# Optimization experiments

Measured on AMD Instinct MI355X. Metric: run time of the kernel, lower is better.

## Reference

```python
import jax, jax.numpy as jnp
import numpy as np

T = 16384      # trajectory length
Z = 8          # num_zones
DIN = 8        # person_attrs_dim
E = 16         # num edges
PENALTY = 1000.0
DIFFUSION_STRENGTH = 0.2
EPS = 1e-20


def setup_inputs() -> dict:
    key = jax.random.key(0)
    ks = jax.random.split(key, 20)
    s = 0.05  # weight scale
    return {
        "person_attrs": jax.random.normal(ks[0], (DIN,), jnp.float32),
        "times": jnp.arange(T, dtype=jnp.float32),
        "gumbel_u": jax.random.uniform(ks[1], (T, Z), jnp.float32),
        "edge_index": jax.random.randint(ks[2], (2, E), 0, Z),
        "W1": jax.random.normal(ks[3], (256, DIN + 1 + Z), jnp.float32) * s,
        "b1": jnp.zeros((256,), jnp.float32),
        "W2": jax.random.normal(ks[4], (128, 256), jnp.float32) * s,
        "b2": jnp.zeros((128,), jnp.float32),
        "W3": jax.random.normal(ks[5], (64, 128), jnp.float32) * s,
        "b3": jnp.zeros((64,), jnp.float32),
        "W4": jax.random.normal(ks[6], (Z, 64), jnp.float32) * s,
        "b4": jnp.zeros((Z,), jnp.float32),
        "D1": jax.random.normal(ks[7], (128, DIN + 1), jnp.float32) * s,
        "d1": jnp.zeros((128,), jnp.float32),
        "D2": jax.random.normal(ks[8], (64, 128), jnp.float32) * s,
        "d2": jnp.zeros((64,), jnp.float32),
        "D3": jax.random.normal(ks[9], (Z, 64), jnp.float32) * s,
        "d3": jnp.zeros((Z,), jnp.float32),
        "tau": jnp.asarray(1.0, jnp.float32),
    }


def _adjacency(edge_index, num_zones):
    A = jnp.zeros((num_zones, num_zones), jnp.float32)
    A = A.at[edge_index[0], edge_index[1]].set(1.0)
    A = A.at[edge_index[1], edge_index[0]].set(1.0)
    d = jnp.arange(num_zones)
    return A.at[d, d].set(1.0)


def _forward(person_attrs, times, gumbel_u, W1, b1, W2, b2, W3, b3, W4, b4,
             D1, d1, D2, d2, D3, d3, tau, edge_index):
    num_zones = W4.shape[0]
    din = person_attrs.shape[0]
    A = _adjacency(edge_index, num_zones)

    # normalized time: times / times[-1] if times[-1] > 0 else 0
    last = times[-1]
    denom = jnp.where(last > 0, last, jnp.asarray(1.0, times.dtype))
    norm_t = jnp.where(last > 0, times / denom, jnp.zeros_like(times))  # [T]

    # Precompute (attrs, time)-dependent parts batched over all timesteps.
    # trajectory_net layer 1 split: columns [0:din]=attrs, [din]=time, [din+1:]=zone one-hot
    f_base = person_attrs @ W1[:, :din].T + norm_t[:, None] * W1[:, din][None, :] + b1  # [T,256]
    W1z = W1[:, din + 1:]  # [256, Z]

    # diversity_net depends only on (attrs, time): batch it fully.
    h = jax.nn.relu(person_attrs @ D1[:, :din].T + norm_t[:, None] * D1[:, din][None, :] + d1)  # [T,128]
    h = jax.nn.relu(h @ D2.T + d2)                                                              # [T,64]
    diversity = jnp.tanh(h @ D3.T + d3)                                                         # [T,Z]

    gumbels = -jnp.log(-jnp.log(gumbel_u + EPS) + EPS)  # [T,Z]

    zone0 = jax.nn.one_hot(0, num_zones, dtype=jnp.float32)

    def step(zone_soft, xs):
        f1, dv, g = xs
        h1 = jax.nn.relu(f1 + W1z @ zone_soft)
        h2 = jax.nn.relu(W2 @ h1 + b2)
        h3 = jax.nn.relu(W3 @ h2 + b3)
        base_logits = W4 @ h3 + b4
        combined = base_logits + DIFFUSION_STRENGTH * dv
        cur = jnp.argmax(zone_soft)
        constrained = combined - PENALTY * (1.0 - A[cur])
        y = jax.nn.softmax((constrained + g) / tau)
        nxt = jnp.argmax(y)
        hard = jax.nn.one_hot(nxt, num_zones, dtype=y.dtype)
        zone_next = y + jax.lax.stop_gradient(hard - y)  # straight-through hard gumbel
        return zone_next, (constrained, nxt)

    _, (traj_logits, traj_zones) = jax.lax.scan(step, zone0, (f_base, diversity, gumbels))
    return traj_logits, traj_zones


def reference(person_attrs, times, gumbel_u, edge_index, W1, b1, W2, b2, W3, b3,
              W4, b4, D1, d1, D2, d2, D3, d3, tau):
    return _forward(person_attrs, times, gumbel_u, W1, b1, W2, b2, W3, b3, W4, b4,
                    D1, d1, D2, d2, D3, d3, tau, edge_index)
```

## Files before the change

### kernel.cpp

```cpp
#include <hip/hip_runtime.h>
#include <cstdint>

#define T_STEPS 16384

#define WS_U     0
#define WS_V     256
#define WS_W1ZT  512
#define WS_PEN   2560
#define WS_A     2624
#define WS_W4T   2688
#define WS_W2T   3968
#define WS_W3T   36736
#define WS_DV    53120
#define WS_G     184192
#define WS_CONS  315264
#define WS_ABT   1363840
#define WS_A4LR  1888128
#define WS_H3LR  1920896
#define WS_END_F 2183040
#define WSB_NXT8 ((size_t)WS_END_F * 4)
#define WSB_CUR  (WSB_NXT8 + 131072)
#define WSB_CRX  (WSB_CUR + 65536)

#define PB_DIV   0
#define PB_W2T   256
#define PB_W3T   (PB_W2T + 128)
#define PB_GUM   (PB_W3T + 32)
#define PB_SETUP (PB_GUM + 512)
#define NB_PREP  (PB_SETUP + 1)

__device__ __forceinline__ unsigned int fn_compose(unsigned int hi, unsigned int lo) {
  unsigned int r = 0;
  #pragma unroll
  for (int x = 0; x < 8; ++x) {
    unsigned int m = (lo >> (3 * x)) & 7u;
    r |= ((hi >> (3 * m)) & 7u) << (3 * x);
  }
  return r;
}

__global__ void __launch_bounds__(256) k_prepdiv(
    const float* __restrict__ pa, const float* __restrict__ times,
    const float* __restrict__ gum, const int* __restrict__ edge,
    const float* __restrict__ W1, const float* __restrict__ b1,
    const float* __restrict__ W2, const float* __restrict__ W3,
    const float* __restrict__ W4,
    const float* __restrict__ D1, const float* __restrict__ d1,
    const float* __restrict__ D2, const float* __restrict__ d2,
    const float* __restrict__ D3, const float* __restrict__ d3,
    float* __restrict__ ws) {
  __shared__ float sD2[64 * 128];
  __shared__ float sudc[128], svdc[128];
  __shared__ float part[3][8][64];
  int b = blockIdx.x, tid = threadIdx.x;
  if (b < PB_W2T) {
    int lane = tid & 63;
    int w = __builtin_amdgcn_readfirstlane(tid >> 6);
    int t = b * 64 + lane;
    float last = times[T_STEPS - 1];
    float st = (last > 0.0f) ? times[t] / last : 0.0f;
    #pragma unroll
    for (int i = 0; i < 8; ++i)
      ((float4*)sD2)[i * 256 + tid] = ((const float4*)D2)[i * 256 + tid];
    if (tid < 128) {
      float acc = d1[tid];
      #pragma unroll
      for (int i = 0; i < 8; ++i) acc = fmaf(pa[i], D1[tid * 9 + i], acc);
      sudc[tid] = acc;
      svdc[tid] = D1[tid * 9 + 8];
    }
    __syncthreads();
    int j0 = __builtin_amdgcn_readfirstlane(w * 16);
    float accj[16];
    #pragma unroll
    for (int jj = 0; jj < 16; ++jj) accj[jj] = d2[j0 + jj];
    #pragma unroll 4
    for (int k = 0; k < 128; ++k) {
      float h1 = fmaxf(fmaf(st, svdc[k], sudc[k]), 0.0f);
      #pragma unroll
      for (int jj = 0; jj < 16; ++jj)
        accj[jj] = fmaf(sD2[(j0 + jj) * 128 + k], h1, accj[jj]);
    }
    float dvp[8];
    #pragma unroll
    for (int z = 0; z < 8; ++z) dvp[z] = (w == 0) ? d3[z] : 0.0f;
    #pragma unroll
    for (int jj = 0; jj < 16; ++jj) {
      float h2 = fmaxf(accj[jj], 0.0f);
      #pragma unroll
      for (int z = 0; z < 8; ++z)
        dvp[z] = fmaf(D3[z * 64 + j0 + jj], h2, dvp[z]);
    }
    if (w > 0) {
      #pragma unroll
      for (int z = 0; z < 8; ++z) part[w - 1][z][lane] = dvp[z];
    }
    __syncthreads();
    if (w == 0) {
      #pragma unroll
      for (int z = 0; z < 8; ++z) {
        float dvv = dvp[z] + part[0][z][lane] + part[1][z][lane] + part[2][z][lane];
        ws[WS_DV + t * 8 + z] = tanhf(dvv);
      }
    }
  } else if (b < PB_W3T) {
    int e = (b - PB_W2T) * 256 + tid;
    int k = e >> 7, j = e & 127;
    ws[WS_W2T + e] = W2[j * 256 + k];
  } else if (b < PB_GUM) {
    int e = (b - PB_W3T) * 256 + tid;
    int i = e & 63, j = e >> 6;
    ws[WS_W3T + e] = W3[i * 128 + j];
  } else if (b < PB_SETUP) {
    int e = (b - PB_GUM) * 256 + tid;
    float uu = gum[e];
    ws[WS_G + e] = -logf(-logf(uu + 1e-20f) + 1e-20f);
  } else {
    {
      int k = tid;
      float acc = b1[k];
      #pragma unroll
      for (int i = 0; i < 8; ++i) acc = fmaf(pa[i], W1[k * 17 + i], acc);
      ws[WS_U + k] = acc;
      ws[WS_V + k] = W1[k * 17 + 8];
    }
    for (int e = tid; e < 2048; e += 256) {
      int cc = e >> 8, k = e & 255;
      ws[WS_W1ZT + e] = W1[k * 17 + 9 + cc];
    }
    for (int e = tid; e < 512; e += 256) {
      int k = e >> 3, z = e & 7;
      ws[WS_W4T + e] = W4[z * 64 + k];
    }
    if (tid < 64) ws[WS_A + tid] = ((tid >> 3) == (tid & 7)) ? 1.0f : 0.0f;
    __syncthreads();
    if (tid == 0) {
      for (int e = 0; e < 16; ++e) {
        int aa = edge[e], bb = edge[16 + e];
        ws[WS_A + aa * 8 + bb] = 1.0f;
        ws[WS_A + bb * 8 + aa] = 1.0f;
      }
    }
    __syncthreads();
    if (tid < 64) ws[WS_PEN + tid] = 1000.0f * (1.0f - ws[WS_A + tid]);
  }
}

__global__ void __launch_bounds__(256) k_ab4(
    const float* __restrict__ times,
    const float* __restrict__ u_, const float* __restrict__ v_,
    const float* __restrict__ w1zt, const float* __restrict__ w2t,
    const float* __restrict__ w3t, const float* __restrict__ w4t,
    const float* __restrict__ b2, const float* __restrict__ b3,
    const float* __restrict__ b4,
    float* __restrict__ abt, int* __restrict__ crx,
    float* __restrict__ a4lr, float* __restrict__ h3lr) {
  __shared__ float s_au[256], s_av[256];
  __shared__ float s_pa[128], s_pb[128];
  __shared__ unsigned long long s_bal[4];
  __shared__ unsigned long long s_bal2[2];
  __shared__ float s_h2L[128], s_h2R[128];
  __shared__ float s_h3pL[4][64], s_h3pR[4][64];
  __shared__ float s_h3L[64], s_h3R[64];
  __shared__ int s_d3, s_cnt, s_cnt2;
  int blk = blockIdx.x;
  int c = blk >> 8, tile = blk & 255;
  int tid = threadIdx.x;
  float last = times[T_STEPS - 1];
  float stL = (last > 0.0f) ? times[tile * 64] / last : 0.0f;
  float stR = (last > 0.0f) ? times[tile * 64 + 63] / last : 0.0f;
  {
    float uk = u_[tid] + w1zt[c * 256 + tid];
    float vk = v_[tid];
    float valL = fmaf(stL, vk, uk);
    float valR = fmaf(stR, vk, uk);
    float mn = fminf(valL, valR);
    float mx = fmaxf(valL, valR);
    bool act = (mn > 0.0f);
    bool cross = (!act) && (mx > 0.0f);
    s_au[tid] = act ? uk : 0.0f;
    s_av[tid] = act ? vk : 0.0f;
    unsigned long long bal = __ballot(cross);
    if ((tid & 63) == 0) s_bal[tid >> 6] = bal;
  }
  if (tid == 0) s_d3 = 0;
  __syncthreads();
  if (tid == 0) {
    int cnt = 0;
    int list8[8];
    #pragma unroll
    for (int i = 0; i < 8; ++i) list8[i] = 0;
    #pragma unroll
    for (int w = 0; w < 4; ++w) {
      unsigned long long m = s_bal[w];
      while (m) {
        int bit = __ffsll(m) - 1;
        if (cnt < 8) list8[cnt] = w * 64 + bit;
        ++cnt;
        m &= (m - 1);
      }
    }
    crx[blk * 24] = cnt;
    s_cnt = cnt;
    #pragma unroll
    for (int i = 0; i < 8; ++i) crx[blk * 24 + 1 + i] = list8[i];
  }
  {
    int j = tid & 127, half = tid >> 7;
    float A = 0.0f, B = 0.0f;
    const float* wrow = w2t + half * 128 * 128 + j;
    int kb = half * 128;
    #pragma unroll 4
    for (int kk = 0; kk < 128; ++kk) {
      float w = wrow[kk * 128];
      A = fmaf(s_au[kb + kk], w, A);
      B = fmaf(s_av[kb + kk], w, B);
    }
    if (half == 1) { s_pa[j] = A; s_pb[j] = B; }
    __syncthreads();
    bool jcross = false;
    if (half == 0) {
      float Af = A + s_pa[j] + b2[j];
      float Bf = B + s_pb[j];
      abt[(size_t)blk * 256 + j * 2]     = Af;
      abt[(size_t)blk * 256 + j * 2 + 1] = Bf;
      float preL = fmaf(stL, Bf, Af);
      float preR = fmaf(stR, Bf, Af);
      jcross = (preL > 0.0f) != (preR > 0.0f);
      s_h2L[j] = fmaxf(preL, 0.0f);
      s_h2R[j] = fmaxf(preR, 0.0f);
    }
    unsigned long long bal2 = __ballot(jcross);
    if ((tid & 63) == 0 && tid < 128) s_bal2[tid >> 6] = bal2;
  }
  __syncthreads();
  if (tid == 0) {
    int cnt2 = 0;
    int list8[8];
    #pragma unroll
    for (int i = 0; i < 8; ++i) list8[i] = 0;
    #pragma unroll
    for (int w = 0; w < 2; ++w) {
      unsigned long long m = s_bal2[w];
      while (m) {
        int bit = __ffsll(m) - 1;
        if (cnt2 < 8) list8[cnt2] = w * 64 + bit;
        ++cnt2;
        m &= (m - 1);
      }
    }
    crx[blk * 24 + 10] = cnt2;
    s_cnt2 = cnt2;
    #pragma unroll
    for (int i = 0; i < 8; ++i) crx[blk * 24 + 11 + i] = list8[i];
  }
  __syncthreads();
  {
    int i = tid & 63, jq = tid >> 6;
    float aL = (jq == 0) ? b3[i] : 0.0f;
    float aR = aL;
    int j0 = jq * 32;
    #pragma unroll 4
    for (int jj = 0; jj < 32; ++jj) {
      float w = w3t[(j0 + jj) * 64 + i];
      aL = fmaf(w, s_h2L[j0 + jj], aL);
      aR = fmaf(w, s_h2R[j0 + jj], aR);
    }
    s_h3pL[jq][i] = aL;
    s_h3pR[jq][i] = aR;
  }
  __syncthreads();
  if (tid < 64) {
    float preL = s_h3pL[0][tid] + s_h3pL[1][tid] + s_h3pL[2][tid] + s_h3pL[3][tid];
    float preR = s_h3pR[0][tid] + s_h3pR[1][tid] + s_h3pR[2][tid] + s_h3pR[3][tid];
    if ((preL > 0.0f) != (preR > 0.0f)) atomicOr(&s_d3, 1);
    s_h3L[tid] = fmaxf(preL, 0.0f);
    s_h3R[tid] = fmaxf(preR, 0.0f);
    h3lr[(size_t)blk * 128 + tid]      = preL;
    h3lr[(size_t)blk * 128 + 64 + tid] = preR;
  }
  __syncthreads();
  if (tid < 8) {
    float aL = b4[tid], aR = b4[tid];
    #pragma unroll 8
    for (int i = 0; i < 64; ++i) {
      float w = w4t[i * 8 + tid];
      aL = fmaf(w, s_h3L[i], aL);
      aR = fmaf(w, s_h3R[i], aR);
    }
    a4lr[blk * 16 + tid]     = aL;
    a4lr[blk * 16 + 8 + tid] = aR;
  }
  if (tid == 0) {
    int flag;
    if (s_cnt > 0 || s_cnt2 > 8) flag = 0;
    else if (s_cnt2 > 0 || s_d3) flag = 3;
    else flag = 1;
    crx[blk * 24 + 9] = flag;
  }
}

__global__ void __launch_bounds__(256, 4) k_mlp(
    const float* __restrict__ times,
    const float* __restrict__ u_, const float* __restrict__ v_,
    const float* __restrict__ w1zt, const float* __restrict__ w2t,
    const float* __restrict__ abt, const int* __restrict__ crx,
    const float* __restrict__ a4lr, const float* __restrict__ h3lr,
    const float* __restrict__ w3t, const float* __restrict__ w4t,
    const float* __restrict__ b2, const float* __restrict__ b3,
    const float* __restrict__ b4,
    const float* __restrict__ dv, const float* __restrict__ gt,
    const float* __restrict__ pen, const float* __restrict__ tau,
    float* __restrict__ cons_out, unsigned char* __restrict__ nxt_out) {
  __shared__ float part[3][8][64];
  __shared__ float s_w3[8192];
  __shared__ float s_ab[256];
  int tid = threadIdx.x;
  int lane = tid & 63;
  int iq = __builtin_amdgcn_readfirstlane(tid >> 6);
  int blk = blockIdx.x;
  int c = blk >> 8, tgrp = blk & 255;
  int t = tgrp * 64 + lane;
  int abase = blk * 256;
  int cbase = blk * 24;
  int flag = crx[cbase + 9];

  if (flag == 1) {
    if (iq == 0) {
      float frac = (float)lane * (1.0f / 63.0f);
      float a4[8];
      #pragma unroll
      for (int z = 0; z < 8; ++z) {
        float L = a4lr[blk * 16 + z];
        float R = a4lr[blk * 16 + 8 + z];
        a4[z] = fmaf(frac, R - L, L);
      }
      float4 dv0 = *(const float4*)(dv + (size_t)t * 8);
      float4 dv1 = *(const float4*)(dv + (size_t)t * 8 + 4);
      float4 g0  = *(const float4*)(gt + (size_t)t * 8);
      float4 g1  = *(const float4*)(gt + (size_t)t * 8 + 4);
      float dvv[8] = {dv0.x, dv0.y, dv0.z, dv0.w, dv1.x, dv1.y, dv1.z, dv1.w};
      float gv[8]  = {g0.x, g0.y, g0.z, g0.w, g1.x, g1.y, g1.z, g1.w};
      float sgn = (tau[0] > 0.0f) ? 1.0f : -1.0f;
      float cons[8];
      float best = 0.0f; int bz = 0;
      #pragma unroll
      for (int z = 0; z < 8; ++z) {
        float lg = fmaf(0.2f, dvv[z], a4[z]) - pen[c * 8 + z];
        cons[z] = lg;
        float yv = (lg + gv[z]) * sgn;
        if (z == 0) { best = yv; bz = 0; }
        else if (yv > best) { best = yv; bz = z; }
      }
      float* co = cons_out + ((size_t)t * 8 + c) * 8;
      *(float4*)co = make_float4(cons[0], cons[1], cons[2], cons[3]);
      *(float4*)(co + 4) = make_float4(cons[4], cons[5], cons[6], cons[7]);
      nxt_out[t * 8 + c] = (unsigned char)bz;
    }
    return;
  }

  float last = times[T_STEPS - 1];
  float st = (last > 0.0f) ? times[t] / last : 0.0f;
  const float* w1c = w1zt + c * 256;
  int cnt = crx[cbase];
  int i0 = iq * 16;

  float acc[16];
  if (flag == 3) {
    float frac = (float)lane * (1.0f / 63.0f);
    #pragma unroll
    for (int i = 0; i < 16; ++i) {
      float L = h3lr[(size_t)blk * 128 + i0 + i];
      float R = h3lr[(size_t)blk * 128 + 64 + i0 + i];
      acc[i] = fmaf(frac, R - L, L);
    }
    int cnt2 = crx[cbase + 10];
    float stL = (last > 0.0f) ? times[tgrp * 64] / last : 0.0f;
    float stR = (last > 0.0f) ? times[tgrp * 64 + 63] / last : 0.0f;
    for (int q = 0; q < cnt2; ++q) {
      int j = crx[cbase + 11 + q];
      float A = abt[abase + j * 2];
      float B = abt[abase + j * 2 + 1];
      float preL = fmaf(stL, B, A);
      float preR = fmaf(stR, B, A);
      float rL = fmaxf(preL, 0.0f);
      float rR = fmaxf(preR, 0.0f);
      float pre = fmaf(st, B, A);
      float corr = fmaxf(pre, 0.0f) - fmaf(frac, rR - rL, rL);
      #pragma unroll
      for (int i = 0; i < 16; ++i)
        acc[i] = fmaf(corr, w3t[j * 64 + i0 + i], acc[i]);
    }
  } else {
    {
      const float4* w3v = (const float4*)w3t;
      float4* sw3 = (float4*)s_w3;
      #pragma unroll
      for (int r = 0; r < 8; ++r) sw3[r * 256 + tid] = w3v[r * 256 + tid];
      s_ab[tid] = abt[abase + tid];
    }
    __syncthreads();
    #pragma unroll
    for (int i = 0; i < 16; ++i) acc[i] = b3[i0 + i];

    if (cnt <= 8) {
      int kk[8];
      #pragma unroll
      for (int i = 0; i < 8; ++i) kk[i] = (i < cnt) ? crx[cbase + 1 + i] : 0;
      float hx[8];
      #pragma unroll
      for (int i = 0; i < 8; ++i)
        hx[i] = (i < cnt) ? fmaxf(fmaf(st, v_[kk[i]], u_[kk[i]] + w1c[kk[i]]), 0.0f) : 0.0f;
      #pragma unroll 2
      for (int j = 0; j < 128; ++j) {
        float2 ab = *(const float2*)(s_ab + j * 2);
        float h2p = fmaf(st, ab.y, ab.x);
        #pragma unroll
        for (int i = 0; i < 8; ++i)
          h2p = fmaf(hx[i], w2t[kk[i] * 128 + j], h2p);
        float h2 = fmaxf(h2p, 0.0f);
        const float4* w3p = (const float4*)(s_w3 + j * 64 + i0);
        float4 w0 = w3p[0], w1 = w3p[1], w2v = w3p[2], w3v = w3p[3];
        acc[0]  = fmaf(w0.x, h2, acc[0]);   acc[1]  = fmaf(w0.y, h2, acc[1]);
        acc[2]  = fmaf(w0.z, h2, acc[2]);   acc[3]  = fmaf(w0.w, h2, acc[3]);
        acc[4]  = fmaf(w1.x, h2, acc[4]);   acc[5]  = fmaf(w1.y, h2, acc[5]);
        acc[6]  = fmaf(w1.z, h2, acc[6]);   acc[7]  = fmaf(w1.w, h2, acc[7]);
        acc[8]  = fmaf(w2v.x, h2, acc[8]);  acc[9]  = fmaf(w2v.y, h2, acc[9]);
        acc[10] = fmaf(w2v.z, h2, acc[10]); acc[11] = fmaf(w2v.w, h2, acc[11]);
        acc[12] = fmaf(w3v.x, h2, acc[12]); acc[13] = fmaf(w3v.y, h2, acc[13]);
        acc[14] = fmaf(w3v.z, h2, acc[14]); acc[15] = fmaf(w3v.w, h2, acc[15]);
      }
    } else {
      for (int j = 0; j < 128; ++j) {
        float h2p = b2[j];
        for (int k = 0; k < 256; ++k) {
          float h1 = fmaxf(fmaf(st, v_[k], u_[k] + w1c[k]), 0.0f);
          h2p = fmaf(w2t[k * 128 + j], h1, h2p);
        }
        float h2 = fmaxf(h2p, 0.0f);
        #pragma unroll
        for (int i = 0; i < 16; ++i)
          acc[i] = fmaf(s_w3[j * 64 + i0 + i], h2, acc[i]);
      }
    }
  }

  float p[8];
  #pragma unroll
  for (int z = 0; z < 8; ++z) p[z] = (iq == 0) ? b4[z] : 0.0f;
  #pragma unroll 4
  for (int i = 0; i < 16; ++i) {
    float h3 = fmaxf(acc[i], 0.0f);
    #pragma unroll
    for (int z = 0; z < 8; ++z)
      p[z] = fmaf(w4t[(i0 + i) * 8 + z], h3, p[z]);
  }
  if (iq > 0) {
    #pragma unroll
    for (int z = 0; z < 8; ++z) part[iq - 1][z][lane] = p[z];
  }
  __syncthreads();
  if (iq == 0) {
    float a4[8];
    #pragma unroll
    for (int z = 0; z < 8; ++z)
      a4[z] = p[z] + part[0][z][lane] + part[1][z][lane] + part[2][z][lane];
    float4 dv0 = *(const float4*)(dv + (size_t)t * 8);
    float4 dv1 = *(const float4*)(dv + (size_t)t * 8 + 4);
    float4 g0  = *(const float4*)(gt + (size_t)t * 8);
    float4 g1  = *(const float4*)(gt + (size_t)t * 8 + 4);
    float dvv[8] = {dv0.x, dv0.y, dv0.z, dv0.w, dv1.x, dv1.y, dv1.z, dv1.w};
    float gv[8]  = {g0.x, g0.y, g0.z, g0.w, g1.x, g1.y, g1.z, g1.w};
    float sgn = (tau[0] > 0.0f) ? 1.0f : -1.0f;
    float cons[8];
    float best = 0.0f; int bz = 0;
    #pragma unroll
    for (int z = 0; z < 8; ++z) {
      float lg = fmaf(0.2f, dvv[z], a4[z]) - pen[c * 8 + z];
      cons[z] = lg;
      float yv = (lg + gv[z]) * sgn;
      if (z == 0) { best = yv; bz = 0; }
      else if (yv > best) { best = yv; bz = z; }
    }
    float* co = cons_out + ((size_t)t * 8 + c) * 8;
    *(float4*)co = make_float4(cons[0], cons[1], cons[2], cons[3]);
    *(float4*)(co + 4) = make_float4(cons[4], cons[5], cons[6], cons[7]);
    nxt_out[t * 8 + c] = (unsigned char)bz;
  }
}

__global__ void __launch_bounds__(1024) k_scangather(const float* __restrict__ ws,
                                                     float* __restrict__ d_out) {
  __shared__ unsigned int sc[1024];
  __shared__ unsigned char cur_s[128];
  int tid = threadIdx.x;
  int bid = blockIdx.x;
  const unsigned char* nxt8 = (const unsigned char*)ws + WSB_NXT8;
  const unsigned int IDENT = 0x00FAC688u;
  unsigned int f[16];
  int t0 = tid * 16;
  unsigned int F = IDENT;
  #pragma unroll
  for (int i = 0; i < 16; ++i) {
    uint2 b = *(const uint2*)(nxt8 + (size_t)(t0 + i) * 8);
    unsigned int fn = 0;
    #pragma unroll
    for (int q = 0; q < 4; ++q) fn |= ((b.x >> (8 * q)) & 7u) << (3 * q);
    #pragma unroll
    for (int q = 0; q < 4; ++q) fn |= ((b.y >> (8 * q)) & 7u) << (3 * (q + 4));
    f[i] = fn;
    F = fn_compose(fn, F);
  }
  sc[tid] = F;
  __syncthreads();
  #pragma unroll
  for (int d = 1; d < 1024; d <<= 1) {
    unsigned int v = sc[tid];
    unsigned int p = (tid >= d) ? sc[tid - d] : 0u;
    unsigned int nv = (tid >= d) ? fn_compose(v, p) : v;
    __syncthreads();
    sc[tid] = nv;
    __syncthreads();
  }
  unsigned int E = (tid == 0) ? IDENT : sc[tid - 1];
  unsigned int state = E & 7u;
  bool mine = (tid >> 3) == bid;
  #pragma unroll
  for (int i = 0; i < 16; ++i) {
    int tt = t0 + i;
    unsigned int nx = (f[i] >> (3 * state)) & 7u;
    if (mine) {
      cur_s[tt - bid * 128] = (unsigned char)state;
      d_out[131072 + tt] = (float)nx;
    }
    state = nx;
  }
  __syncthreads();
  int idx = bid * 1024 + tid;
  int t = idx >> 3, z = idx & 7;
  unsigned int cur = cur_s[t - bid * 128];
  d_out[idx] = ws[WS_CONS + ((size_t)t * 8 + (int)cur) * 8 + z];
}

extern "C" void kernel_launch(void* const* d_in, const int* in_sizes, int n_in,
                              void* d_out, int out_size, void* d_ws, size_t ws_size,
                              hipStream_t stream) {
  const float* pa    = (const float*)d_in[0];
  const float* times = (const float*)d_in[1];
  const float* gum   = (const float*)d_in[2];
  const int*   edge  = (const int*)d_in[3];
  const float* W1  = (const float*)d_in[4];
  const float* b1  = (const float*)d_in[5];
  const float* W2  = (const float*)d_in[6];
  const float* b2  = (const float*)d_in[7];
  const float* W3  = (const float*)d_in[8];
  const float* b3  = (const float*)d_in[9];
  const float* W4  = (const float*)d_in[10];
  const float* b4  = (const float*)d_in[11];
  const float* D1  = (const float*)d_in[12];
  const float* d1v = (const float*)d_in[13];
  const float* D2  = (const float*)d_in[14];
  const float* d2v = (const float*)d_in[15];
  const float* D3  = (const float*)d_in[16];
  const float* d3v = (const float*)d_in[17];
  const float* tau = (const float*)d_in[18];
  float* ws = (float*)d_ws;
  float* out = (float*)d_out;
  int* crx = (int*)((char*)d_ws + WSB_CRX);

  k_prepdiv<<<NB_PREP, 256, 0, stream>>>(pa, times, gum, edge, W1, b1, W2, W3, W4,
                                         D1, d1v, D2, d2v, D3, d3v, ws);
  k_ab4<<<2048, 256, 0, stream>>>(times, ws + WS_U, ws + WS_V, ws + WS_W1ZT,
                                  ws + WS_W2T, ws + WS_W3T, ws + WS_W4T,
                                  b2, b3, b4, ws + WS_ABT, crx,
                                  ws + WS_A4LR, ws + WS_H3LR);
  k_mlp<<<2048, 256, 0, stream>>>(times, ws + WS_U, ws + WS_V, ws + WS_W1ZT,
                                  ws + WS_W2T, ws + WS_ABT, crx,
                                  ws + WS_A4LR, ws + WS_H3LR,
                                  ws + WS_W3T, ws + WS_W4T, b2, b3, b4,
                                  ws + WS_DV, ws + WS_G, ws + WS_PEN, tau,
                                  ws + WS_CONS, (unsigned char*)ws + WSB_NXT8);
  k_scangather<<<128, 1024, 0, stream>>>(ws, out);
}
```

Measured before the change: 79.15 us.

## Move diversity and gumbel work into ab kernel; recompute linear-tile logits in gather

The diversity MLP and the gumbel transform move out of the small prep kernel into the large ab kernel as extra blocks, sharing shared memory through a union, and the D2 staging is split into two halves to cut LDS use. This shortens the serial prep launch and lets that work overlap with the ab tiles. The fast linear-tile path in the MLP kernel no longer writes the full 8x8 constrained logits per step. The gather kernel instead rebuilds the needed row from the tile endpoint logits, the diversity term and the penalty when the tile flag says the tile is linear. This trades a large write for extra reads and branching in the final gather.

```diff
diff --git a/kernel.cpp b/kernel.cpp
--- a/kernel.cpp
+++ b/kernel.cpp
@@ -19,15 +19,13 @@
 #define WS_H3LR  1920896
 #define WS_END_F 2183040
 #define WSB_NXT8 ((size_t)WS_END_F * 4)
-#define WSB_CUR  (WSB_NXT8 + 131072)
-#define WSB_CRX  (WSB_CUR + 65536)
-
-#define PB_DIV   0
-#define PB_W2T   256
-#define PB_W3T   (PB_W2T + 128)
-#define PB_GUM   (PB_W3T + 32)
-#define PB_SETUP (PB_GUM + 512)
-#define NB_PREP  (PB_SETUP + 1)
+#define WSB_CRX  (WSB_NXT8 + 131072 + 65536)
+
+#define NB_PREP  161
+#define AB_N     2048
+#define DIVB     2048
+#define GUMB     (DIVB + 256)
+#define NB_ABDG  (GUMB + 512)
 
 __device__ __forceinline__ unsigned int fn_compose(unsigned int hi, unsigned int lo) {
   unsigned int r = 0;
@@ -39,82 +37,21 @@
   return r;
 }
 
-__global__ void __launch_bounds__(256) k_prepdiv(
-    const float* __restrict__ pa, const float* __restrict__ times,
-    const float* __restrict__ gum, const int* __restrict__ edge,
+__global__ void __launch_bounds__(256) k_prep(
+    const float* __restrict__ pa, const int* __restrict__ edge,
     const float* __restrict__ W1, const float* __restrict__ b1,
     const float* __restrict__ W2, const float* __restrict__ W3,
     const float* __restrict__ W4,
-    const float* __restrict__ D1, const float* __restrict__ d1,
-    const float* __restrict__ D2, const float* __restrict__ d2,
-    const float* __restrict__ D3, const float* __restrict__ d3,
     float* __restrict__ ws) {
-  __shared__ float sD2[64 * 128];
-  __shared__ float sudc[128], svdc[128];
-  __shared__ float part[3][8][64];
   int b = blockIdx.x, tid = threadIdx.x;
-  if (b < PB_W2T) {
-    int lane = tid & 63;
-    int w = __builtin_amdgcn_readfirstlane(tid >> 6);
-    int t = b * 64 + lane;
-    float last = times[T_STEPS - 1];
-    float st = (last > 0.0f) ? times[t] / last : 0.0f;
-    #pragma unroll
-    for (int i = 0; i < 8; ++i)
-      ((float4*)sD2)[i * 256 + tid] = ((const float4*)D2)[i * 256 + tid];
-    if (tid < 128) {
-      float acc = d1[tid];
-      #pragma unroll
-      for (int i = 0; i < 8; ++i) acc = fmaf(pa[i], D1[tid * 9 + i], acc);
-      sudc[tid] = acc;
-      svdc[tid] = D1[tid * 9 + 8];
-    }
-    __syncthreads();
-    int j0 = __builtin_amdgcn_readfirstlane(w * 16);
-    float accj[16];
-    #pragma unroll
-    for (int jj = 0; jj < 16; ++jj) accj[jj] = d2[j0 + jj];
-    #pragma unroll 4
-    for (int k = 0; k < 128; ++k) {
-      float h1 = fmaxf(fmaf(st, svdc[k], sudc[k]), 0.0f);
-      #pragma unroll
-      for (int jj = 0; jj < 16; ++jj)
-        accj[jj] = fmaf(sD2[(j0 + jj) * 128 + k], h1, accj[jj]);
-    }
-    float dvp[8];
-    #pragma unroll
-    for (int z = 0; z < 8; ++z) dvp[z] = (w == 0) ? d3[z] : 0.0f;
-    #pragma unroll
-    for (int jj = 0; jj < 16; ++jj) {
-      float h2 = fmaxf(accj[jj], 0.0f);
-      #pragma unroll
-      for (int z = 0; z < 8; ++z)
-        dvp[z] = fmaf(D3[z * 64 + j0 + jj], h2, dvp[z]);
-    }
-    if (w > 0) {
-      #pragma unroll
-      for (int z = 0; z < 8; ++z) part[w - 1][z][lane] = dvp[z];
-    }
-    __syncthreads();
-    if (w == 0) {
-      #pragma unroll
-      for (int z = 0; z < 8; ++z) {
-        float dvv = dvp[z] + part[0][z][lane] + part[1][z][lane] + part[2][z][lane];
-        ws[WS_DV + t * 8 + z] = tanhf(dvv);
-      }
-    }
-  } else if (b < PB_W3T) {
-    int e = (b - PB_W2T) * 256 + tid;
+  if (b < 128) {
+    int e = b * 256 + tid;
     int k = e >> 7, j = e & 127;
     ws[WS_W2T + e] = W2[j * 256 + k];
-  } else if (b < PB_GUM) {
-    int e = (b - PB_W3T) * 256 + tid;
+  } else if (b < 160) {
+    int e = (b - 128) * 256 + tid;
     int i = e & 63, j = e >> 6;
     ws[WS_W3T + e] = W3[i * 128 + j];
-  } else if (b < PB_SETUP) {
-    int e = (b - PB_GUM) * 256 + tid;
-    float uu = gum[e];
-    ws[WS_G + e] = -logf(-logf(uu + 1e-20f) + 1e-20f);
   } else {
     {
       int k = tid;
@@ -146,157 +83,240 @@
   }
 }
 
-__global__ void __launch_bounds__(256) k_ab4(
-    const float* __restrict__ times,
+struct __align__(16) SmemDiv {
+  float sD2h[64 * 64];
+  float sudc[128], svdc[128];
+  float part[3][8][64];
+};
+struct __align__(16) SmemAb {
+  float au[256], av[256];
+  float pa_[128], pb_[128];
+  unsigned long long bal[4];
+  unsigned long long bal2[2];
+  float h2L[128], h2R[128];
+  float h3pL[4][64], h3pR[4][64];
+  float h3L[64], h3R[64];
+  int d3, cnt, cnt2;
+};
+union SmemU {
+  SmemDiv div;
+  SmemAb ab;
+};
+
+__global__ void __launch_bounds__(256) k_abdivg(
+    const float* __restrict__ pa, const float* __restrict__ times,
+    const float* __restrict__ gum,
     const float* __restrict__ u_, const float* __restrict__ v_,
     const float* __restrict__ w1zt, const float* __restrict__ w2t,
     const float* __restrict__ w3t, const float* __restrict__ w4t,
     const float* __restrict__ b2, const float* __restrict__ b3,
     const float* __restrict__ b4,
-    float* __restrict__ abt, int* __restrict__ crx,
+    const float* __restrict__ D1, const float* __restrict__ d1,
+    const float* __restrict__ D2, const float* __restrict__ d2,
+    const float* __restrict__ D3, const float* __restrict__ d3,
+    float* __restrict__ ws, float* __restrict__ abt, int* __restrict__ crx,
     float* __restrict__ a4lr, float* __restrict__ h3lr) {
-  __shared__ float s_au[256], s_av[256];
-  __shared__ float s_pa[128], s_pb[128];
-  __shared__ unsigned long long s_bal[4];
-  __shared__ unsigned long long s_bal2[2];
-  __shared__ float s_h2L[128], s_h2R[128];
-  __shared__ float s_h3pL[4][64], s_h3pR[4][64];
-  __shared__ float s_h3L[64], s_h3R[64];
-  __shared__ int s_d3, s_cnt, s_cnt2;
-  int blk = blockIdx.x;
-  int c = blk >> 8, tile = blk & 255;
-  int tid = threadIdx.x;
+  __shared__ SmemU sm;
+  int bid = blockIdx.x, tid = threadIdx.x;
   float last = times[T_STEPS - 1];
-  float stL = (last > 0.0f) ? times[tile * 64] / last : 0.0f;
-  float stR = (last > 0.0f) ? times[tile * 64 + 63] / last : 0.0f;
-  {
-    float uk = u_[tid] + w1zt[c * 256 + tid];
-    float vk = v_[tid];
-    float valL = fmaf(stL, vk, uk);
-    float valR = fmaf(stR, vk, uk);
-    float mn = fminf(valL, valR);
-    float mx = fmaxf(valL, valR);
-    bool act = (mn > 0.0f);
-    bool cross = (!act) && (mx > 0.0f);
-    s_au[tid] = act ? uk : 0.0f;
-    s_av[tid] = act ? vk : 0.0f;
-    unsigned long long bal = __ballot(cross);
-    if ((tid & 63) == 0) s_bal[tid >> 6] = bal;
-  }
-  if (tid == 0) s_d3 = 0;
-  __syncthreads();
-  if (tid == 0) {
-    int cnt = 0;
-    int list8[8];
-    #pragma unroll
-    for (int i = 0; i < 8; ++i) list8[i] = 0;
-    #pragma unroll
-    for (int w = 0; w < 4; ++w) {
-      unsigned long long m = s_bal[w];
-      while (m) {
-        int bit = __ffsll(m) - 1;
-        if (cnt < 8) list8[cnt] = w * 64 + bit;
-        ++cnt;
-        m &= (m - 1);
-      }
-    }
-    crx[blk * 24] = cnt;
-    s_cnt = cnt;
-    #pragma unroll
-    for (int i = 0; i < 8; ++i) crx[blk * 24 + 1 + i] = list8[i];
-  }
-  {
-    int j = tid & 127, half = tid >> 7;
-    float A = 0.0f, B = 0.0f;
-    const float* wrow = w2t + half * 128 * 128 + j;
-    int kb = half * 128;
-    #pragma unroll 4
-    for (int kk = 0; kk < 128; ++kk) {
-      float w = wrow[kk * 128];
-      A = fmaf(s_au[kb + kk], w, A);
-      B = fmaf(s_av[kb + kk], w, B);
-    }
-    if (half == 1) { s_pa[j] = A; s_pb[j] = B; }
-    __syncthreads();
-    bool jcross = false;
-    if (half == 0) {
-      float Af = A + s_pa[j] + b2[j];
-      float Bf = B + s_pb[j];
-      abt[(size_t)blk * 256 + j * 2]     = Af;
-      abt[(size_t)blk * 256 + j * 2 + 1] = Bf;
-      float preL = fmaf(stL, Bf, Af);
-      float preR = fmaf(stR, Bf, Af);
-      jcross = (preL > 0.0f) != (preR > 0.0f);
-      s_h2L[j] = fmaxf(preL, 0.0f);
-      s_h2R[j] = fmaxf(preR, 0.0f);
-    }
-    unsigned long long bal2 = __ballot(jcross);
-    if ((tid & 63) == 0 && tid < 128) s_bal2[tid >> 6] = bal2;
-  }
-  __syncthreads();
-  if (tid == 0) {
-    int cnt2 = 0;
-    int list8[8];
-    #pragma unroll
-    for (int i = 0; i < 8; ++i) list8[i] = 0;
-    #pragma unroll
-    for (int w = 0; w < 2; ++w) {
-      unsigned long long m = s_bal2[w];
-      while (m) {
-        int bit = __ffsll(m) - 1;
-        if (cnt2 < 8) list8[cnt2] = w * 64 + bit;
-        ++cnt2;
-        m &= (m - 1);
-      }
-    }
-    crx[blk * 24 + 10] = cnt2;
-    s_cnt2 = cnt2;
-    #pragma unroll
-    for (int i = 0; i < 8; ++i) crx[blk * 24 + 11 + i] = list8[i];
-  }
-  __syncthreads();
-  {
-    int i = tid & 63, jq = tid >> 6;
-    float aL = (jq == 0) ? b3[i] : 0.0f;
-    float aR = aL;
-    int j0 = jq * 32;
-    #pragma unroll 4
-    for (int jj = 0; jj < 32; ++jj) {
-      float w = w3t[(j0 + jj) * 64 + i];
-      aL = fmaf(w, s_h2L[j0 + jj], aL);
-      aR = fmaf(w, s_h2R[j0 + jj], aR);
-    }
-    s_h3pL[jq][i] = aL;
-    s_h3pR[jq][i] = aR;
-  }
-  __syncthreads();
-  if (tid < 64) {
-    float preL = s_h3pL[0][tid] + s_h3pL[1][tid] + s_h3pL[2][tid] + s_h3pL[3][tid];
-    float preR = s_h3pR[0][tid] + s_h3pR[1][tid] + s_h3pR[2][tid] + s_h3pR[3][tid];
-    if ((preL > 0.0f) != (preR > 0.0f)) atomicOr(&s_d3, 1);
-    s_h3L[tid] = fmaxf(preL, 0.0f);
-    s_h3R[tid] = fmaxf(preR, 0.0f);
-    h3lr[(size_t)blk * 128 + tid]      = preL;
-    h3lr[(size_t)blk * 128 + 64 + tid] = preR;
-  }
-  __syncthreads();
-  if (tid < 8) {
-    float aL = b4[tid], aR = b4[tid];
-    #pragma unroll 8
-    for (int i = 0; i < 64; ++i) {
-      float w = w4t[i * 8 + tid];
-      aL = fmaf(w, s_h3L[i], aL);
-      aR = fmaf(w, s_h3R[i], aR);
-    }
-    a4lr[blk * 16 + tid]     = aL;
-    a4lr[blk * 16 + 8 + tid] = aR;
-  }
-  if (tid == 0) {
-    int flag;
-    if (s_cnt > 0 || s_cnt2 > 8) flag = 0;
-    else if (s_cnt2 > 0 || s_d3) flag = 3;
-    else flag = 1;
-    crx[blk * 24 + 9] = flag;
+
+  if (bid < AB_N) {
+    int blk = bid;
+    int c = blk >> 8, tile = blk & 255;
+    float stL = (last > 0.0f) ? times[tile * 64] / last : 0.0f;
+    float stR = (last > 0.0f) ? times[tile * 64 + 63] / last : 0.0f;
+    {
+      float uk = u_[tid] + w1zt[c * 256 + tid];
+      float vk = v_[tid];
+      float valL = fmaf(stL, vk, uk);
+      float valR = fmaf(stR, vk, uk);
+      float mn = fminf(valL, valR);
+      float mx = fmaxf(valL, valR);
+      bool act = (mn > 0.0f);
+      bool cross = (!act) && (mx > 0.0f);
+      sm.ab.au[tid] = act ? uk : 0.0f;
+      sm.ab.av[tid] = act ? vk : 0.0f;
+      unsigned long long bal = __ballot(cross);
+      if ((tid & 63) == 0) sm.ab.bal[tid >> 6] = bal;
+    }
+    if (tid == 0) sm.ab.d3 = 0;
+    __syncthreads();
+    if (tid == 0) {
+      int cnt = 0;
+      int list8[8];
+      #pragma unroll
+      for (int i = 0; i < 8; ++i) list8[i] = 0;
+      #pragma unroll
+      for (int w = 0; w < 4; ++w) {
+        unsigned long long m = sm.ab.bal[w];
+        while (m) {
+          int bit = __ffsll(m) - 1;
+          if (cnt < 8) list8[cnt] = w * 64 + bit;
+          ++cnt;
+          m &= (m - 1);
+        }
+      }
+      crx[blk * 24] = cnt;
+      sm.ab.cnt = cnt;
+      #pragma unroll
+      for (int i = 0; i < 8; ++i) crx[blk * 24 + 1 + i] = list8[i];
+    }
+    {
+      int j = tid & 127, half = tid >> 7;
+      float A = 0.0f, B = 0.0f;
+      const float* wrow = w2t + half * 128 * 128 + j;
+      int kb = half * 128;
+      #pragma unroll 4
+      for (int kk = 0; kk < 128; ++kk) {
+        float w = wrow[kk * 128];
+        A = fmaf(sm.ab.au[kb + kk], w, A);
+        B = fmaf(sm.ab.av[kb + kk], w, B);
+      }
+      if (half == 1) { sm.ab.pa_[j] = A; sm.ab.pb_[j] = B; }
+      __syncthreads();
+      bool jcross = false;
+      if (half == 0) {
+        float Af = A + sm.ab.pa_[j] + b2[j];
+        float Bf = B + sm.ab.pb_[j];
+        abt[(size_t)blk * 256 + j * 2]     = Af;
+        abt[(size_t)blk * 256 + j * 2 + 1] = Bf;
+        float preL = fmaf(stL, Bf, Af);
+        float preR = fmaf(stR, Bf, Af);
+        jcross = (preL > 0.0f) != (preR > 0.0f);
+        sm.ab.h2L[j] = fmaxf(preL, 0.0f);
+        sm.ab.h2R[j] = fmaxf(preR, 0.0f);
+      }
+      unsigned long long bal2 = __ballot(jcross);
+      if ((tid & 63) == 0 && tid < 128) sm.ab.bal2[tid >> 6] = bal2;
+    }
+    __syncthreads();
+    if (tid == 0) {
+      int cnt2 = 0;
+      int list8[8];
+      #pragma unroll
+      for (int i = 0; i < 8; ++i) list8[i] = 0;
+      #pragma unroll
+      for (int w = 0; w < 2; ++w) {
+        unsigned long long m = sm.ab.bal2[w];
+        while (m) {
+          int bit = __ffsll(m) - 1;
+          if (cnt2 < 8) list8[cnt2] = w * 64 + bit;
+          ++cnt2;
+          m &= (m - 1);
+        }
+      }
+      crx[blk * 24 + 10] = cnt2;
+      sm.ab.cnt2 = cnt2;
+      #pragma unroll
+      for (int i = 0; i < 8; ++i) crx[blk * 24 + 11 + i] = list8[i];
+    }
+    __syncthreads();
+    {
+      int i = tid & 63, jq = tid >> 6;
+      float aL = (jq == 0) ? b3[i] : 0.0f;
+      float aR = aL;
+      int j0 = jq * 32;
+      #pragma unroll 4
+      for (int jj = 0; jj < 32; ++jj) {
+        float w = w3t[(j0 + jj) * 64 + i];
+        aL = fmaf(w, sm.ab.h2L[j0 + jj], aL);
+        aR = fmaf(w, sm.ab.h2R[j0 + jj], aR);
+      }
+      sm.ab.h3pL[jq][i] = aL;
+      sm.ab.h3pR[jq][i] = aR;
+    }
+    __syncthreads();
+    if (tid < 64) {
+      float preL = sm.ab.h3pL[0][tid] + sm.ab.h3pL[1][tid] + sm.ab.h3pL[2][tid] + sm.ab.h3pL[3][tid];
+      float preR = sm.ab.h3pR[0][tid] + sm.ab.h3pR[1][tid] + sm.ab.h3pR[2][tid] + sm.ab.h3pR[3][tid];
+      if ((preL > 0.0f) != (preR > 0.0f)) atomicOr(&sm.ab.d3, 1);
+      sm.ab.h3L[tid] = fmaxf(preL, 0.0f);
+      sm.ab.h3R[tid] = fmaxf(preR, 0.0f);
+      h3lr[(size_t)blk * 128 + tid]      = preL;
+      h3lr[(size_t)blk * 128 + 64 + tid] = preR;
+    }
+    __syncthreads();
+    if (tid < 8) {
+      float aL = b4[tid], aR = b4[tid];
+      #pragma unroll 8
+      for (int i = 0; i < 64; ++i) {
+        float w = w4t[i * 8 + tid];
+        aL = fmaf(w, sm.ab.h3L[i], aL);
+        aR = fmaf(w, sm.ab.h3R[i], aR);
+      }
+      a4lr[blk * 16 + tid]     = aL;
+      a4lr[blk * 16 + 8 + tid] = aR;
+    }
+    if (tid == 0) {
+      int flag;
+      if (sm.ab.cnt > 0 || sm.ab.cnt2 > 8) flag = 0;
+      else if (sm.ab.cnt2 > 0 || sm.ab.d3) flag = 3;
+      else flag = 1;
+      crx[blk * 24 + 9] = flag;
+    }
+  } else if (bid < GUMB) {
+    int db = bid - DIVB;
+    int lane = tid & 63;
+    int w = __builtin_amdgcn_readfirstlane(tid >> 6);
+    int t = db * 64 + lane;
+    float st = (last > 0.0f) ? times[t] / last : 0.0f;
+    if (tid < 128) {
+      float acc = d1[tid];
+      #pragma unroll
+      for (int i = 0; i < 8; ++i) acc = fmaf(pa[i], D1[tid * 9 + i], acc);
+      sm.div.sudc[tid] = acc;
+      sm.div.svdc[tid] = D1[tid * 9 + 8];
+    }
+    int j0 = __builtin_amdgcn_readfirstlane(w * 16);
+    float accj[16];
+    #pragma unroll
+    for (int jj = 0; jj < 16; ++jj) accj[jj] = d2[j0 + jj];
+    for (int half = 0; half < 2; ++half) {
+      __syncthreads();
+      #pragma unroll
+      for (int r = 0; r < 4; ++r) {
+        int e4 = r * 256 + tid;
+        int j = e4 >> 4, kk4 = e4 & 15;
+        ((float4*)sm.div.sD2h)[e4] =
+            *(const float4*)(D2 + j * 128 + half * 64 + kk4 * 4);
+      }
+      __syncthreads();
+      #pragma unroll 4
+      for (int kk = 0; kk < 64; ++kk) {
+        int k = half * 64 + kk;
+        float h1 = fmaxf(fmaf(st, sm.div.svdc[k], sm.div.sudc[k]), 0.0f);
+        #pragma unroll
+        for (int jj = 0; jj < 16; ++jj)
+          accj[jj] = fmaf(sm.div.sD2h[(j0 + jj) * 64 + kk], h1, accj[jj]);
+      }
+    }
+    float dvp[8];
+    #pragma unroll
+    for (int z = 0; z < 8; ++z) dvp[z] = (w == 0) ? d3[z] : 0.0f;
+    #pragma unroll
+    for (int jj = 0; jj < 16; ++jj) {
+      float h2 = fmaxf(accj[jj], 0.0f);
+      #pragma unroll
+      for (int z = 0; z < 8; ++z)
+        dvp[z] = fmaf(D3[z * 64 + j0 + jj], h2, dvp[z]);
+    }
+    if (w > 0) {
+      #pragma unroll
+      for (int z = 0; z < 8; ++z) sm.div.part[w - 1][z][lane] = dvp[z];
+    }
+    __syncthreads();
+    if (w == 0) {
+      #pragma unroll
+      for (int z = 0; z < 8; ++z) {
+        float dvv = dvp[z] + sm.div.part[0][z][lane] + sm.div.part[1][z][lane] +
+                    sm.div.part[2][z][lane];
+        ws[WS_DV + t * 8 + z] = tanhf(dvv);
+      }
+    }
+  } else {
+    int e = (bid - GUMB) * 256 + tid;
+    float uu = gum[e];
+    ws[WS_G + e] = -logf(-logf(uu + 1e-20f) + 1e-20f);
   }
 }
 
@@ -342,19 +362,14 @@
       float dvv[8] = {dv0.x, dv0.y, dv0.z, dv0.w, dv1.x, dv1.y, dv1.z, dv1.w};
       float gv[8]  = {g0.x, g0.y, g0.z, g0.w, g1.x, g1.y, g1.z, g1.w};
       float sgn = (tau[0] > 0.0f) ? 1.0f : -1.0f;
-      float cons[8];
       float best = 0.0f; int bz = 0;
       #pragma unroll
       for (int z = 0; z < 8; ++z) {
         float lg = fmaf(0.2f, dvv[z], a4[z]) - pen[c * 8 + z];
-        cons[z] = lg;
         float yv = (lg + gv[z]) * sgn;
         if (z == 0) { best = yv; bz = 0; }
         else if (yv > best) { best = yv; bz = z; }
       }
-      float* co = cons_out + ((size_t)t * 8 + c) * 8;
-      *(float4*)co = make_float4(cons[0], cons[1], cons[2], cons[3]);
-      *(float4*)(co + 4) = make_float4(cons[4], cons[5], cons[6], cons[7]);
       nxt_out[t * 8 + c] = (unsigned char)bz;
     }
     return;
@@ -490,8 +505,10 @@
   }
 }
 
-__global__ void __launch_bounds__(1024) k_scangather(const float* __restrict__ ws,
-                                                     float* __restrict__ d_out) {
+__global__ void __launch_bounds__(1024) k_scangather(
+    const float* __restrict__ ws, const int* __restrict__ crx,
+    const float* __restrict__ a4lr, const float* __restrict__ dv,
+    const float* __restrict__ pen, float* __restrict__ d_out) {
   __shared__ unsigned int sc[1024];
   __shared__ unsigned char cur_s[128];
   int tid = threadIdx.x;
@@ -539,8 +556,21 @@
   __syncthreads();
   int idx = bid * 1024 + tid;
   int t = idx >> 3, z = idx & 7;
-  unsigned int cur = cur_s[t - bid * 128];
-  d_out[idx] = ws[WS_CONS + ((size_t)t * 8 + (int)cur) * 8 + z];
+  int cur = (int)cur_s[t - bid * 128];
+  int tile = t >> 6;
+  int blk2 = cur * 256 + tile;
+  int flag = crx[blk2 * 24 + 9];
+  float val;
+  if (flag == 1) {
+    float frac = (float)(t & 63) * (1.0f / 63.0f);
+    float L = a4lr[blk2 * 16 + z];
+    float R = a4lr[blk2 * 16 + 8 + z];
+    float a4 = fmaf(frac, R - L, L);
+    val = fmaf(0.2f, dv[(size_t)t * 8 + z], a4) - pen[cur * 8 + z];
+  } else {
+    val = ws[WS_CONS + ((size_t)t * 8 + cur) * 8 + z];
+  }
+  d_out[idx] = val;
 }
 
 extern "C" void kernel_launch(void* const* d_in, const int* in_sizes, int n_in,
@@ -569,17 +599,19 @@
   float* out = (float*)d_out;
   int* crx = (int*)((char*)d_ws + WSB_CRX);
 
-  k_prepdiv<<<NB_PREP, 256, 0, stream>>>(pa, times, gum, edge, W1, b1, W2, W3, W4,
-                                         D1, d1v, D2, d2v, D3, d3v, ws);
-  k_ab4<<<2048, 256, 0, stream>>>(times, ws + WS_U, ws + WS_V, ws + WS_W1ZT,
-                                  ws + WS_W2T, ws + WS_W3T, ws + WS_W4T,
-                                  b2, b3, b4, ws + WS_ABT, crx,
-                                  ws + WS_A4LR, ws + WS_H3LR);
+  k_prep<<<NB_PREP, 256, 0, stream>>>(pa, edge, W1, b1, W2, W3, W4, ws);
+  k_abdivg<<<NB_ABDG, 256, 0, stream>>>(pa, times, gum,
+                                        ws + WS_U, ws + WS_V, ws + WS_W1ZT,
+                                        ws + WS_W2T, ws + WS_W3T, ws + WS_W4T,
+                                        b2, b3, b4, D1, d1v, D2, d2v, D3, d3v,
+                                        ws, ws + WS_ABT, crx,
+                                        ws + WS_A4LR, ws + WS_H3LR);
   k_mlp<<<2048, 256, 0, stream>>>(times, ws + WS_U, ws + WS_V, ws + WS_W1ZT,
                                   ws + WS_W2T, ws + WS_ABT, crx,
                                   ws + WS_A4LR, ws + WS_H3LR,
                                   ws + WS_W3T, ws + WS_W4T, b2, b3, b4,
                                   ws + WS_DV, ws + WS_G, ws + WS_PEN, tau,
                                   ws + WS_CONS, (unsigned char*)ws + WSB_NXT8);
-  k_scangather<<<128, 1024, 0, stream>>>(ws, out);
+  k_scangather<<<128, 1024, 0, stream>>>(ws, crx, ws + WS_A4LR, ws + WS_DV,
+                                         ws + WS_PEN, out);
 }
```

After: 86.89 us. 9.8% more time.
